# Performance work log

Hardware: AMD Instinct MI355X
Metric: run time of the kernel (lower is better)

Reference implementation:

```python
import jax, jax.numpy as jnp
import numpy as np
import math

RAND_N = 32
B = 262144
MAX_DEG = 9
P = MAX_DEG + 1  # padded Legendre polynomial length
EPS = 1e-8


def _rot_xyz(a, b, c):
    # scipy Rotation.from_euler('xyz', [a,b,c]) (extrinsic): R = Rz(c) @ Ry(b) @ Rx(a)
    ca, sa = math.cos(a), math.sin(a)
    cb, sb = math.cos(b), math.sin(b)
    cc, sc = math.cos(c), math.sin(c)
    Rx = np.array([[1, 0, 0], [0, ca, -sa], [0, sa, ca]])
    Ry = np.array([[cb, 0, sb], [0, 1, 0], [-sb, 0, cb]])
    Rz = np.array([[cc, -sc, 0], [sc, cc, 0], [0, 0, 1]])
    return Rz @ Ry @ Rx


def setup_inputs() -> dict:
    key = jax.random.key(0)
    k1, k2 = jax.random.split(key)
    rng = np.random.default_rng(0)

    # random rotation matrices (buffer 'matrices')
    angs = rng.random((RAND_N, 3)) * 2.0 * np.pi
    matrices = np.stack([_rot_xyz(*a) for a in angs]).astype(np.float32)

    # degrees ~ N(0,10) clipped to [1,9], int (buffer 'degrees')
    degs = np.clip(rng.normal(0.0, 10.0, (RAND_N,)), 1, 9).astype(np.int32)

    # per-basis Legendre coeffs (increasing power, zero-padded) + scalar constants
    coeffs_pad = np.zeros((RAND_N, P), np.float32)
    coeff_scale = np.zeros((RAND_N,), np.float32)
    y0_norm = np.zeros((RAND_N,), np.float32)
    for i, l in enumerate(degs):
        l = int(l)
        c = np.polynomial.legendre.leg2poly(np.eye(l + 1)[l])  # == scipy legendre(l).c[::-1]
        coeffs_pad[i, : l + 1] = c
        logc = -2 * math.log(l) - math.lgamma(l + 1) + 0.5 * (math.lgamma(2 * l + 2) - math.log(4 * math.pi))
        coeff_scale[i] = ((-1) ** l) * math.exp(logc)
        y0_norm[i] = math.sqrt((2 * l + 1) / (4 * math.pi))

    vec = jax.random.normal(k1, (B, 3), jnp.float32)
    vec = vec / jnp.linalg.norm(vec, axis=-1, keepdims=True)  # unit directions
    roughness = jax.random.uniform(k2, (B, 1), jnp.float32, 0.01, 1.0)

    return {
        "vec": vec,
        "roughness": roughness,
        "matrices": jnp.asarray(matrices),
        "coeffs_pad": jnp.asarray(coeffs_pad),
        "coeff_scale": jnp.asarray(coeff_scale),
        "y0_norm": jnp.asarray(y0_norm),
        "degrees": jnp.asarray(degs),
    }


def reference(vec, roughness, matrices, coeffs_pad, coeff_scale, y0_norm, degrees):
    # vec: (B,3), roughness: (B,1)
    kappa = 1.0 / (roughness + EPS)                          # (B,1)
    rvec = jnp.einsum('bi,nij->bnj', vec, matrices)          # (B,N,3) all bases at once
    x_, y_, z_ = rvec[..., 0], rvec[..., 1], rvec[..., 2]
    phi = jnp.arctan2(y_, x_)                                # (B,N)
    theta = jnp.arctan2(z_, jnp.sqrt(x_ * x_ + y_ * y_)) - jnp.pi / 2

    # ragged-degree Legendre power series, padded to P terms
    ct = jnp.cos(theta)                                      # (B,N)
    powers = jnp.arange(P)                                   # (P,) int exponents
    v = jnp.einsum('bnp,np->bn', ct[..., None] ** powers, coeffs_pad)
    y0 = y0_norm * v                                         # (B,N)

    # real part of coeff * sin(theta)^deg * exp(i*deg*phi)  (deg>=1 so ind=1 branch)
    yl1 = coeff_scale * (jnp.sin(theta) ** degrees) * jnp.cos(degrees * phi)

    # Al(l, kappa) = exp(-l(l+1)/2/(kappa+eps)); broadcasts (B,1)x(N,) -> (B,N)
    al = jnp.exp(-(degrees * (degrees + 1)).astype(jnp.float32) * 0.5 / (kappa + EPS))

    out = al[..., None] * jnp.stack([y0, yl1], axis=-1)      # (B,N,2)
    return out.reshape(out.shape[0], -1)                     # (B, 2*N)
```

## Files before the change

kernel.cpp:

```cpp
#include <hip/hip_runtime.h>
#include <math.h>


#define NBASIS 32
#define PLEN 10
#define EPSV 1e-8f
#define LOG2E 1.44269504088896340736f
#define ROWD 65
#define NT 2

typedef float f32x4 __attribute__((ext_vector_type(4)));

__global__ __launch_bounds__(256) void randish_kernel(
    const float* __restrict__ vec,
    const float* __restrict__ rough,
    const float* __restrict__ mats,
    const float* __restrict__ coeffs,
    const float* __restrict__ cscale,
    const float* __restrict__ y0n,
    const int*   __restrict__ degs,
    float* __restrict__ out,
    int B)
{
    __shared__ float lds[64 * ROWD];

    const int t    = threadIdx.x;
    const int lane = t & 63;
    const int w    = t >> 6;

    float V0[NT], V1[NT], V2[NT], TC[NT];
    int   BB[NT];
#pragma unroll
    for (int it = 0; it < NT; ++it) {
        const int b0 = (blockIdx.x * NT + it) * 64;
        const int b  = b0 + lane;
        BB[it] = b0;
        V0[it] = vec[b * 3 + 0];
        V1[it] = vec[b * 3 + 1];
        V2[it] = vec[b * 3 + 2];
        TC[it] = (rough[b] + EPSV) * (-0.5f * LOG2E);
    }

    float* row = &lds[lane * ROWD];

#pragma unroll
    for (int it = 0; it < NT; ++it) {
        const float v0 = V0[it], v1 = V1[it], v2 = V2[it], tc = TC[it];

#pragma unroll
        for (int j = 0; j < 8; ++j) {
            const int n = __builtin_amdgcn_readfirstlane(8 * w + j);
            const int d = __builtin_amdgcn_readfirstlane(degs[n]);

            const float xh = fmaf(v0, mats[n*9+0], fmaf(v1, mats[n*9+3], v2 * mats[n*9+6]));
            const float yh = fmaf(v0, mats[n*9+1], fmaf(v1, mats[n*9+4], v2 * mats[n*9+7]));
            const float ct = fmaf(v0, mats[n*9+2], fmaf(v1, mats[n*9+5], v2 * mats[n*9+8]));

            const float al = __builtin_amdgcn_exp2f((float)(d * (d + 1)) * tc);

            float y0v, yl1v;
            if (d == 1) {
                y0v  = y0n[n] * ct;
                yl1v = -cscale[n] * xh;
            } else {
                const int par  = d & 1;
                const int base = n * PLEN + par;
                const float ct2 = ct * ct;

                const int K = d >> 1;
                float v;
                if (K == 1) {
                    v = fmaf(coeffs[base+2], ct2, coeffs[base]);
                } else if (K == 2) {
                    v = fmaf(coeffs[base+4], ct2, coeffs[base+2]);
                    v = fmaf(v, ct2, coeffs[base]);
                } else if (K == 3) {
                    v = fmaf(coeffs[base+6], ct2, coeffs[base+4]);
                    v = fmaf(v, ct2, coeffs[base+2]);
                    v = fmaf(v, ct2, coeffs[base]);
                } else {
                    v = fmaf(coeffs[base+8], ct2, coeffs[base+6]);
                    v = fmaf(v, ct2, coeffs[base+4]);
                    v = fmaf(v, ct2, coeffs[base+2]);
                    v = fmaf(v, ct2, coeffs[base]);
                }
                if (par) v *= ct;

                const float ss  = fmaf(yh, yh, xh * xh);
                const float m2x = xh + xh;
                float Rm2 = 1.0f, Rm1 = xh;
                for (int k = 2; k <= d; ++k) {
                    const float Rk = fmaf(m2x, Rm1, -(ss * Rm2));
                    Rm2 = Rm1;
                    Rm1 = Rk;
                }
                float cs = cscale[n];
                if (par) cs = -cs;

                y0v  = y0n[n] * v;
                yl1v = cs * Rm1;
            }

            row[2 * n + 0] = al * y0v;
            row[2 * n + 1] = al * yl1v;
        }

        __syncthreads();

        f32x4 o[4];
#pragma unroll
        for (int p = 0; p < 4; ++p) {
            const int c  = p * 256 + t;
            const int r  = c >> 4;
            const int c4 = (c & 15) * 4;
            const float* src = &lds[r * ROWD + c4];
            o[p] = f32x4{ src[0], src[1], src[2], src[3] };
        }
        f32x4* outp = reinterpret_cast<f32x4*>(out + (size_t)BB[it] * 64);
#pragma unroll
        for (int p = 0; p < 4; ++p)
            __builtin_nontemporal_store(o[p], outp + p * 256 + t);

        if (it + 1 < NT) __syncthreads();
    }
}

extern "C" void kernel_launch(void* const* d_in, const int* in_sizes, int n_in,
                              void* d_out, int out_size, void* d_ws, size_t ws_size,
                              hipStream_t stream) {
    const float* vec    = (const float*)d_in[0];
    const float* rough  = (const float*)d_in[1];
    const float* mats   = (const float*)d_in[2];
    const float* coeffs = (const float*)d_in[3];
    const float* cscale = (const float*)d_in[4];
    const float* y0n    = (const float*)d_in[5];
    const int*   degs   = (const int*)d_in[6];
    float* out = (float*)d_out;

    const int B = in_sizes[1];
    const int block = 256;
    const int grid = B / (64 * NT);

    randish_kernel<<<grid, block, 0, stream>>>(vec, rough, mats, coeffs, cscale,
                                               y0n, degs, out, B);
}
```

Before: 20.37 us.

## Warp-specialize producer and store waves with double-buffered LDS tiles

Splits each block into two compute waves and two store waves. The compute waves each handle 16 bases per tile and write into one of two alternating LDS buffers. The store waves stream the previous tile to global memory with nontemporal stores. Each block now processes four tiles instead of two, so the grid is half as large. The goal is to overlap the ALU-heavy basis evaluation with the output writes, at the cost of half as many lanes doing the arithmetic and extra barrier synchronisation.

```diff
diff --git a/kernel.cpp b/kernel.cpp
--- a/kernel.cpp
+++ b/kernel.cpp
@@ -7,7 +7,12 @@
 #define EPSV 1e-8f
 #define LOG2E 1.44269504088896340736f
 #define ROWD 65
-#define NT 2
+#define NTILE 4
+
+#define BAR_LDS()  do {                                           \
+    asm volatile("s_waitcnt lgkmcnt(0)" ::: "memory");            \
+    __builtin_amdgcn_s_barrier();                                 \
+} while (0)
 
 typedef float f32x4 __attribute__((ext_vector_type(4)));
 
@@ -22,106 +27,116 @@
     float* __restrict__ out,
     int B)
 {
-    __shared__ float lds[64 * ROWD];
+    __shared__ float lds[2][64 * ROWD];
 
     const int t    = threadIdx.x;
     const int lane = t & 63;
-    const int w    = t >> 6;
+    const int wid  = t >> 6;
 
-    float V0[NT], V1[NT], V2[NT], TC[NT];
-    int   BB[NT];
+    if (wid < 2) {
+        const int p = wid;
+
+        float V0[NTILE], V1[NTILE], V2[NTILE], TC[NTILE];
 #pragma unroll
-    for (int it = 0; it < NT; ++it) {
-        const int b0 = (blockIdx.x * NT + it) * 64;
-        const int b  = b0 + lane;
-        BB[it] = b0;
-        V0[it] = vec[b * 3 + 0];
-        V1[it] = vec[b * 3 + 1];
-        V2[it] = vec[b * 3 + 2];
-        TC[it] = (rough[b] + EPSV) * (-0.5f * LOG2E);
-    }
-
-    float* row = &lds[lane * ROWD];
-
-#pragma unroll
-    for (int it = 0; it < NT; ++it) {
-        const float v0 = V0[it], v1 = V1[it], v2 = V2[it], tc = TC[it];
-
-#pragma unroll
-        for (int j = 0; j < 8; ++j) {
-            const int n = __builtin_amdgcn_readfirstlane(8 * w + j);
-            const int d = __builtin_amdgcn_readfirstlane(degs[n]);
-
-            const float xh = fmaf(v0, mats[n*9+0], fmaf(v1, mats[n*9+3], v2 * mats[n*9+6]));
-            const float yh = fmaf(v0, mats[n*9+1], fmaf(v1, mats[n*9+4], v2 * mats[n*9+7]));
-            const float ct = fmaf(v0, mats[n*9+2], fmaf(v1, mats[n*9+5], v2 * mats[n*9+8]));
-
-            const float al = __builtin_amdgcn_exp2f((float)(d * (d + 1)) * tc);
-
-            float y0v, yl1v;
-            if (d == 1) {
-                y0v  = y0n[n] * ct;
-                yl1v = -cscale[n] * xh;
-            } else {
-                const int par  = d & 1;
-                const int base = n * PLEN + par;
-                const float ct2 = ct * ct;
-
-                const int K = d >> 1;
-                float v;
-                if (K == 1) {
-                    v = fmaf(coeffs[base+2], ct2, coeffs[base]);
-                } else if (K == 2) {
-                    v = fmaf(coeffs[base+4], ct2, coeffs[base+2]);
-                    v = fmaf(v, ct2, coeffs[base]);
-                } else if (K == 3) {
-                    v = fmaf(coeffs[base+6], ct2, coeffs[base+4]);
-                    v = fmaf(v, ct2, coeffs[base+2]);
-                    v = fmaf(v, ct2, coeffs[base]);
-                } else {
-                    v = fmaf(coeffs[base+8], ct2, coeffs[base+6]);
-                    v = fmaf(v, ct2, coeffs[base+4]);
-                    v = fmaf(v, ct2, coeffs[base+2]);
-                    v = fmaf(v, ct2, coeffs[base]);
-                }
-                if (par) v *= ct;
-
-                const float ss  = fmaf(yh, yh, xh * xh);
-                const float m2x = xh + xh;
-                float Rm2 = 1.0f, Rm1 = xh;
-                for (int k = 2; k <= d; ++k) {
-                    const float Rk = fmaf(m2x, Rm1, -(ss * Rm2));
-                    Rm2 = Rm1;
-                    Rm1 = Rk;
-                }
-                float cs = cscale[n];
-                if (par) cs = -cs;
-
-                y0v  = y0n[n] * v;
-                yl1v = cs * Rm1;
-            }
-
-            row[2 * n + 0] = al * y0v;
-            row[2 * n + 1] = al * yl1v;
+        for (int it = 0; it < NTILE; ++it) {
+            const int b = (blockIdx.x * NTILE + it) * 64 + lane;
+            V0[it] = vec[b * 3 + 0];
+            V1[it] = vec[b * 3 + 1];
+            V2[it] = vec[b * 3 + 2];
+            TC[it] = (rough[b] + EPSV) * (-0.5f * LOG2E);
         }
 
-        __syncthreads();
+        auto compute_tile = [&](int it, int buf) {
+            const float v0 = V0[it], v1 = V1[it], v2 = V2[it], tc = TC[it];
+            float* row = &lds[buf][lane * ROWD];
+#pragma unroll
+            for (int j = 0; j < 16; ++j) {
+                const int n = __builtin_amdgcn_readfirstlane(16 * p + j);
+                const int d = __builtin_amdgcn_readfirstlane(degs[n]);
 
-        f32x4 o[4];
+                const float xh = fmaf(v0, mats[n*9+0], fmaf(v1, mats[n*9+3], v2 * mats[n*9+6]));
+                const float yh = fmaf(v0, mats[n*9+1], fmaf(v1, mats[n*9+4], v2 * mats[n*9+7]));
+                const float ct = fmaf(v0, mats[n*9+2], fmaf(v1, mats[n*9+5], v2 * mats[n*9+8]));
+
+                const float al = __builtin_amdgcn_exp2f((float)(d * (d + 1)) * tc);
+
+                float y0v, yl1v;
+                if (d == 1) {
+                    y0v  = y0n[n] * ct;
+                    yl1v = -cscale[n] * xh;
+                } else {
+                    const int par  = d & 1;
+                    const int base = n * PLEN + par;
+                    const float ct2 = ct * ct;
+                    const int K = d >> 1;
+                    float v;
+                    if (K == 1) {
+                        v = fmaf(coeffs[base+2], ct2, coeffs[base]);
+                    } else if (K == 2) {
+                        v = fmaf(coeffs[base+4], ct2, coeffs[base+2]);
+                        v = fmaf(v, ct2, coeffs[base]);
+                    } else if (K == 3) {
+                        v = fmaf(coeffs[base+6], ct2, coeffs[base+4]);
+                        v = fmaf(v, ct2, coeffs[base+2]);
+                        v = fmaf(v, ct2, coeffs[base]);
+                    } else {
+                        v = fmaf(coeffs[base+8], ct2, coeffs[base+6]);
+                        v = fmaf(v, ct2, coeffs[base+4]);
+                        v = fmaf(v, ct2, coeffs[base+2]);
+                        v = fmaf(v, ct2, coeffs[base]);
+                    }
+                    if (par) v *= ct;
+
+                    const float ss  = fmaf(yh, yh, xh * xh);
+                    const float m2x = xh + xh;
+                    float Rm2 = 1.0f, Rm1 = xh;
+                    for (int k = 2; k <= d; ++k) {
+                        const float Rk = fmaf(m2x, Rm1, -(ss * Rm2));
+                        Rm2 = Rm1;
+                        Rm1 = Rk;
+                    }
+                    float cs = cscale[n];
+                    if (par) cs = -cs;
+                    y0v  = y0n[n] * v;
+                    yl1v = cs * Rm1;
+                }
+                row[2 * n + 0] = al * y0v;
+                row[2 * n + 1] = al * yl1v;
+            }
+        };
+
+        compute_tile(0, 0);
+        BAR_LDS();
 #pragma unroll
-        for (int p = 0; p < 4; ++p) {
-            const int c  = p * 256 + t;
-            const int r  = c >> 4;
-            const int c4 = (c & 15) * 4;
-            const float* src = &lds[r * ROWD + c4];
-            o[p] = f32x4{ src[0], src[1], src[2], src[3] };
+        for (int it = 0; it < NTILE - 1; ++it) {
+            compute_tile(it + 1, (it + 1) & 1);
+            BAR_LDS();
         }
-        f32x4* outp = reinterpret_cast<f32x4*>(out + (size_t)BB[it] * 64);
+    } else {
+        const int cl = t - 128;
+
+        BAR_LDS();
+        f32x4 oA[8], oB[8];
 #pragma unroll
-        for (int p = 0; p < 4; ++p)
-            __builtin_nontemporal_store(o[p], outp + p * 256 + t);
+        for (int it = 0; it < NTILE; ++it) {
+            f32x4* o = (it & 1) ? oB : oA;
+            const int buf = it & 1;
+#pragma unroll
+            for (int k = 0; k < 8; ++k) {
+                const int c  = k * 128 + cl;
+                const int r  = c >> 4;
+                const int c4 = (c & 15) * 4;
+                const float* src = &lds[buf][r * ROWD + c4];
+                o[k] = f32x4{ src[0], src[1], src[2], src[3] };
+            }
+            f32x4* outp = reinterpret_cast<f32x4*>(
+                out + (size_t)(blockIdx.x * NTILE + it) * 64 * 64);
+#pragma unroll
+            for (int k = 0; k < 8; ++k)
+                __builtin_nontemporal_store(o[k], outp + k * 128 + cl);
 
-        if (it + 1 < NT) __syncthreads();
+            if (it < NTILE - 1) BAR_LDS();
+        }
     }
 }
 
@@ -139,7 +154,7 @@
 
     const int B = in_sizes[1];
     const int block = 256;
-    const int grid = B / (64 * NT);
+    const int grid = B / (64 * NTILE);
 
     randish_kernel<<<grid, block, 0, stream>>>(vec, rough, mats, coeffs, cscale,
                                                y0n, degs, out, B);
```

New measurement: 27.87 us. 1.37x slower.
